# Optimization experiments

Measured on AMD Instinct MI355X. Metric: run time of the kernel, lower is better.

Reference implementation:

```python
import jax, jax.numpy as jnp
import numpy as np

B, N, D_IN, D_OUT = 8, 2048, 128, 64
NEG_INF = -9e15
LEAKY_ALPHA = 0.2


def setup_inputs() -> dict:
    key = jax.random.key(0)
    k_h, k_adj, k_w, k_a = jax.random.split(key, 4)
    h = jax.random.normal(k_h, (B, N, D_IN), dtype=jnp.float32)
    # sparse-ish 0/1 adjacency with forced self-loops (diagonal ones)
    adj = (jax.random.uniform(k_adj, (B, N, N)) < 0.02).astype(jnp.float32)
    adj = jnp.maximum(adj, jnp.eye(N, dtype=jnp.float32)[None, :, :])
    # glorot uniform init for w and a
    lim_w = np.sqrt(6.0 / (D_IN + D_OUT))
    w = jax.random.uniform(k_w, (D_IN, D_OUT), minval=-lim_w, maxval=lim_w, dtype=jnp.float32)
    lim_a = np.sqrt(6.0 / (2 * D_OUT + 1))
    a = jax.random.uniform(k_a, (2 * D_OUT, 1), minval=-lim_a, maxval=lim_a, dtype=jnp.float32)
    return {"h": h, "adj": adj, "w": w, "a": a}


def reference(h, adj, w, a):
    # wh: (B, N, D_OUT)
    wh = jnp.einsum('bnd,df->bnf', h, w)
    # Split a into the halves acting on source (i) and target (j) features.
    # concat([wh_i, wh_j]) @ a == wh_i @ a1 + wh_j @ a2  (exact same math,
    # avoids materializing the (B,N,N,2F) pairwise tensor).
    f = wh.shape[-1]
    s1 = wh @ a[:f, 0]   # (B, N) -> score contribution of node i (rows)
    s2 = wh @ a[f:, 0]   # (B, N) -> score contribution of node j (cols)
    scores = s1[:, :, None] + s2[:, None, :]            # (B, N, N)
    scores = jnp.where(scores >= 0, scores, LEAKY_ALPHA * scores)  # LeakyReLU(0.2)
    masked = jnp.where(adj > 0, scores, NEG_INF)
    coeffs = jax.nn.softmax(masked, axis=2)             # (B, N, N)
    new_h = jnp.einsum('bij,bjf->bif', coeffs, wh)      # (B, N, D_OUT)
    return new_h
```

## Files before the change

kernel.cpp:

```cpp
#include <hip/hip_runtime.h>
#include <hip/hip_bf16.h>
#include <math.h>


#define GAT_B 8
#define GAT_N 2048
#define GAT_DIN 128
#define GAT_DOUT 64

__global__ __launch_bounds__(256) void gat_wh_kernel(
    const float* __restrict__ h, const float* __restrict__ w,
    const float* __restrict__ a, float* __restrict__ wh,
    float* __restrict__ s1, float* __restrict__ s2) {
  __shared__ float w_lds[GAT_DIN * GAT_DOUT];
  __shared__ float h_lds[4][GAT_DIN];

  for (int t = threadIdx.x; t < (GAT_DIN * GAT_DOUT) / 4; t += 256)
    ((float4*)w_lds)[t] = ((const float4*)w)[t];

  const int lane = threadIdx.x & 63;
  const int wv = threadIdx.x >> 6;
  const float a1 = a[lane];
  const float a2 = a[GAT_DOUT + lane];

  const int ngroups = (GAT_B * GAT_N) / 4;
  for (int rg = blockIdx.x; rg < ngroups; rg += gridDim.x) {
    __syncthreads();
    const float4* hsrc = (const float4*)(h + (size_t)rg * 4 * GAT_DIN);
    for (int t = threadIdx.x; t < (4 * GAT_DIN) / 4; t += 256)
      ((float4*)&h_lds[0][0])[t] = hsrc[t];
    __syncthreads();

    const int row = rg * 4 + wv;
    float acc = 0.f;
#pragma unroll 16
    for (int d = 0; d < GAT_DIN; ++d)
      acc = fmaf(h_lds[wv][d], w_lds[d * GAT_DOUT + lane], acc);

    wh[(size_t)row * GAT_DOUT + lane] = acc;

    float t1 = acc * a1, t2 = acc * a2;
#pragma unroll
    for (int off = 32; off >= 1; off >>= 1) {
      t1 += __shfl_xor(t1, off);
      t2 += __shfl_xor(t2, off);
    }
    if (lane == 0) { s1[row] = t1; s2[row] = t2; }
  }
}

__global__ __launch_bounds__(256) void gat_row_kernel(
    const float* __restrict__ adj, const float* __restrict__ wh,
    const float* __restrict__ s1, const float* __restrict__ s2,
    float* __restrict__ out) {
  __shared__ unsigned int idx_l[4][256];
  __shared__ float sc_l[4][256];

  const int lane = threadIdx.x & 63;
  const int wv = threadIdx.x >> 6;
  const int row = blockIdx.x * 4 + wv;
  const int b = row >> 11;

  const float* adj_row = adj + (size_t)row * GAT_N;
  const float* s2b = s2 + (size_t)b * GAT_N;
  const float* whb = wh + (size_t)b * GAT_N * GAT_DOUT;
  const float s1i = s1[row];
  unsigned int* my_idx = idx_l[wv];
  float* my_sc = sc_l[wv];

  float m = -1e30f;
  float l0 = 0.f, l1 = 0.f;
  float acc0 = 0.f, acc1 = 0.f;

  for (int c = 0; c < GAT_N; c += 256) {
    const float4 av = *(const float4*)(adj_row + c + lane * 4);
    const float4 sv = *(const float4*)(s2b + c + lane * 4);
    int base = 0;
    float cmax = -1e30f;
#pragma unroll
    for (int comp = 0; comp < 4; ++comp) {
      const float a_c = (comp == 0) ? av.x : (comp == 1) ? av.y
                       : (comp == 2) ? av.z : av.w;
      const float s_c = (comp == 0) ? sv.x : (comp == 1) ? sv.y
                       : (comp == 2) ? sv.z : sv.w;
      float sc = s1i + s_c;
      sc = (sc >= 0.f) ? sc : 0.2f * sc;
      const bool pred = a_c > 0.f;
      const unsigned long long msk = __ballot(pred);
      if (msk) {
        const int prefix = __builtin_amdgcn_mbcnt_hi(
            (unsigned)(msk >> 32),
            __builtin_amdgcn_mbcnt_lo((unsigned)msk, 0u));
        if (pred) {
          my_idx[base + prefix] = (unsigned)(c + lane * 4 + comp);
          my_sc[base + prefix] = sc;
          cmax = fmaxf(cmax, sc);
        }
        base += (int)__popcll(msk);
      }
    }
    if (base == 0) continue;

#pragma unroll
    for (int off = 32; off >= 1; off >>= 1)
      cmax = fmaxf(cmax, __shfl_xor(cmax, off));

    const float newm = fmaxf(m, cmax);
    const float r = __expf(m - newm);
    l0 *= r; l1 *= r; acc0 *= r; acc1 *= r;
    m = newm;

    int t = 0;
    for (; t + 2 <= base; t += 2) {
      const float e0 = __expf(my_sc[t] - m);
      const float e1 = __expf(my_sc[t + 1] - m);
      const unsigned j0 = my_idx[t];
      const unsigned j1 = my_idx[t + 1];
      l0 += e0;
      l1 += e1;
      acc0 = fmaf(e0, whb[(size_t)j0 * GAT_DOUT + lane], acc0);
      acc1 = fmaf(e1, whb[(size_t)j1 * GAT_DOUT + lane], acc1);
    }
    if (t < base) {
      const float e0 = __expf(my_sc[t] - m);
      const unsigned j0 = my_idx[t];
      l0 += e0;
      acc0 = fmaf(e0, whb[(size_t)j0 * GAT_DOUT + lane], acc0);
    }
  }
  out[(size_t)row * GAT_DOUT + lane] = (acc0 + acc1) / (l0 + l1);
}

extern "C" void kernel_launch(void* const* d_in, const int* in_sizes, int n_in,
                              void* d_out, int out_size, void* d_ws, size_t ws_size,
                              hipStream_t stream) {
  const float* h   = (const float*)d_in[0];
  const float* adj = (const float*)d_in[1];
  const float* w   = (const float*)d_in[2];
  const float* a   = (const float*)d_in[3];
  float* out = (float*)d_out;

  const size_t rows = (size_t)GAT_B * GAT_N;
  float* wh = (float*)d_ws;
  float* s1 = wh + rows * GAT_DOUT;
  float* s2 = s1 + rows;

  gat_wh_kernel<<<1024, 256, 0, stream>>>(h, w, a, wh, s1, s2);
  gat_row_kernel<<<(GAT_B * GAT_N) / 4, 256, 0, stream>>>(adj, wh, s1, s2, out);
}
```

Measured before the change: 64.16 us.

## Split each attention row across four wavefronts with block-level softmax reduction

Each row is now handled by a whole block instead of one wavefront. Each of the four wavefronts compacts a 512-column slice of the adjacency row, and the max, exp-sum and weighted-sum partials are combined through shared memory. s2 is staged in LDS once per block, and scores are computed only for nonzero columns. This shortens each wavefront's serial chain of gathers and removes online-softmax rescaling, at the cost of four times more blocks, redundant s2 staging per row, and extra barriers.

Measured after the change: 60.18 us. 1.07x faster.

```diff
diff --git a/kernel.cpp b/kernel.cpp
--- a/kernel.cpp
+++ b/kernel.cpp
@@ -53,82 +53,102 @@
     const float* __restrict__ adj, const float* __restrict__ wh,
     const float* __restrict__ s1, const float* __restrict__ s2,
     float* __restrict__ out) {
-  __shared__ unsigned int idx_l[4][256];
-  __shared__ float sc_l[4][256];
+  __shared__ float s2_lds[GAT_N];
+  __shared__ float sc_l[4][512];
+  __shared__ unsigned short idx_l[4][512];
+  __shared__ float acc_l[4][GAT_DOUT];
+  __shared__ float wmax[4];
+  __shared__ float wsum[4];
 
   const int lane = threadIdx.x & 63;
   const int wv = threadIdx.x >> 6;
-  const int row = blockIdx.x * 4 + wv;
+  const int row = blockIdx.x;
   const int b = row >> 11;
 
   const float* adj_row = adj + (size_t)row * GAT_N;
   const float* s2b = s2 + (size_t)b * GAT_N;
   const float* whb = wh + (size_t)b * GAT_N * GAT_DOUT;
   const float s1i = s1[row];
-  unsigned int* my_idx = idx_l[wv];
-  float* my_sc = sc_l[wv];
 
-  float m = -1e30f;
-  float l0 = 0.f, l1 = 0.f;
-  float acc0 = 0.f, acc1 = 0.f;
+  const int c0 = wv * 512;
+  const float4 av0 = *(const float4*)(adj_row + c0 + lane * 4);
+  const float4 av1 = *(const float4*)(adj_row + c0 + 256 + lane * 4);
 
-  for (int c = 0; c < GAT_N; c += 256) {
-    const float4 av = *(const float4*)(adj_row + c + lane * 4);
-    const float4 sv = *(const float4*)(s2b + c + lane * 4);
-    int base = 0;
-    float cmax = -1e30f;
-#pragma unroll
-    for (int comp = 0; comp < 4; ++comp) {
-      const float a_c = (comp == 0) ? av.x : (comp == 1) ? av.y
-                       : (comp == 2) ? av.z : av.w;
-      const float s_c = (comp == 0) ? sv.x : (comp == 1) ? sv.y
-                       : (comp == 2) ? sv.z : sv.w;
-      float sc = s1i + s_c;
-      sc = (sc >= 0.f) ? sc : 0.2f * sc;
-      const bool pred = a_c > 0.f;
-      const unsigned long long msk = __ballot(pred);
-      if (msk) {
-        const int prefix = __builtin_amdgcn_mbcnt_hi(
-            (unsigned)(msk >> 32),
-            __builtin_amdgcn_mbcnt_lo((unsigned)msk, 0u));
-        if (pred) {
-          my_idx[base + prefix] = (unsigned)(c + lane * 4 + comp);
-          my_sc[base + prefix] = sc;
-          cmax = fmaxf(cmax, sc);
-        }
-        base += (int)__popcll(msk);
+  {
+    const float4* src = (const float4*)s2b;
+    float4* dst = (float4*)s2_lds;
+    dst[threadIdx.x] = src[threadIdx.x];
+    dst[threadIdx.x + 256] = src[threadIdx.x + 256];
+  }
+  __syncthreads();
+
+  int base = 0;
+  float cmax = -1e30f;
+  auto compact = [&](float a_c, int j) {
+    const bool pred = a_c > 0.f;
+    const unsigned long long msk = __ballot(pred);
+    if (msk) {
+      const int prefix = __builtin_amdgcn_mbcnt_hi(
+          (unsigned)(msk >> 32),
+          __builtin_amdgcn_mbcnt_lo((unsigned)msk, 0u));
+      if (pred) {
+        float sc = s1i + s2_lds[j];
+        sc = (sc >= 0.f) ? sc : 0.2f * sc;
+        sc_l[wv][base + prefix] = sc;
+        idx_l[wv][base + prefix] = (unsigned short)j;
+        cmax = fmaxf(cmax, sc);
       }
+      base += (int)__popcll(msk);
     }
-    if (base == 0) continue;
+  };
+  compact(av0.x, c0 + lane * 4 + 0);
+  compact(av0.y, c0 + lane * 4 + 1);
+  compact(av0.z, c0 + lane * 4 + 2);
+  compact(av0.w, c0 + lane * 4 + 3);
+  compact(av1.x, c0 + 256 + lane * 4 + 0);
+  compact(av1.y, c0 + 256 + lane * 4 + 1);
+  compact(av1.z, c0 + 256 + lane * 4 + 2);
+  compact(av1.w, c0 + 256 + lane * 4 + 3);
 
 #pragma unroll
-    for (int off = 32; off >= 1; off >>= 1)
-      cmax = fmaxf(cmax, __shfl_xor(cmax, off));
+  for (int off = 32; off >= 1; off >>= 1)
+    cmax = fmaxf(cmax, __shfl_xor(cmax, off));
+  if (lane == 0) wmax[wv] = cmax;
+  __syncthreads();
 
-    const float newm = fmaxf(m, cmax);
-    const float r = __expf(m - newm);
-    l0 *= r; l1 *= r; acc0 *= r; acc1 *= r;
-    m = newm;
+  const float m = fmaxf(fmaxf(wmax[0], wmax[1]), fmaxf(wmax[2], wmax[3]));
 
-    int t = 0;
-    for (; t + 2 <= base; t += 2) {
-      const float e0 = __expf(my_sc[t] - m);
-      const float e1 = __expf(my_sc[t + 1] - m);
-      const unsigned j0 = my_idx[t];
-      const unsigned j1 = my_idx[t + 1];
-      l0 += e0;
-      l1 += e1;
-      acc0 = fmaf(e0, whb[(size_t)j0 * GAT_DOUT + lane], acc0);
-      acc1 = fmaf(e1, whb[(size_t)j1 * GAT_DOUT + lane], acc1);
-    }
-    if (t < base) {
-      const float e0 = __expf(my_sc[t] - m);
-      const unsigned j0 = my_idx[t];
-      l0 += e0;
-      acc0 = fmaf(e0, whb[(size_t)j0 * GAT_DOUT + lane], acc0);
-    }
+  float l0 = 0.f, l1 = 0.f, acc0 = 0.f, acc1 = 0.f;
+  const float* scw = sc_l[wv];
+  const unsigned short* idxw = idx_l[wv];
+  int t = 0;
+  for (; t + 2 <= base; t += 2) {
+    const float e0 = __expf(scw[t] - m);
+    const float e1 = __expf(scw[t + 1] - m);
+    const int j0 = idxw[t];
+    const int j1 = idxw[t + 1];
+    l0 += e0;
+    l1 += e1;
+    acc0 = fmaf(e0, whb[(size_t)j0 * GAT_DOUT + lane], acc0);
+    acc1 = fmaf(e1, whb[(size_t)j1 * GAT_DOUT + lane], acc1);
   }
-  out[(size_t)row * GAT_DOUT + lane] = (acc0 + acc1) / (l0 + l1);
+  if (t < base) {
+    const float e0 = __expf(scw[t] - m);
+    const int j0 = idxw[t];
+    l0 += e0;
+    acc0 = fmaf(e0, whb[(size_t)j0 * GAT_DOUT + lane], acc0);
+  }
+
+  acc_l[wv][lane] = acc0 + acc1;
+  if (lane == 0) wsum[wv] = l0 + l1;
+  __syncthreads();
+
+  if (wv == 0) {
+    const float acc = acc_l[0][lane] + acc_l[1][lane] +
+                      acc_l[2][lane] + acc_l[3][lane];
+    const float l = wsum[0] + wsum[1] + wsum[2] + wsum[3];
+    out[(size_t)row * GAT_DOUT + lane] = acc / l;
+  }
 }
 
 extern "C" void kernel_launch(void* const* d_in, const int* in_sizes, int n_in,
@@ -146,5 +166,5 @@
   float* s2 = s1 + rows;
 
   gat_wh_kernel<<<1024, 256, 0, stream>>>(h, w, a, wh, s1, s2);
-  gat_row_kernel<<<(GAT_B * GAT_N) / 4, 256, 0, stream>>>(adj, wh, s1, s2, out);
+  gat_row_kernel<<<GAT_B * GAT_N, 256, 0, stream>>>(adj, wh, s1, s2, out);
 }
```
